# Kernel tuning notes

Measured on AMD Instinct MI355X. Metric: run time of the kernel, lower is better.

The kernel has to match this reference:

```python
import jax, jax.numpy as jnp
import numpy as np

B_SZ, N_NODES, C_IN, C_OUT, M_EDGES, DEG = 32, 4096, 64, 64, 64, 256
E_INC = M_EDGES * DEG  # 16384 incidences
NEG_SLOPE = 0.2
MARGIN = 4.2


def setup_inputs() -> dict:
    key = jax.random.key(0)
    k1, k2, k3, k4 = jax.random.split(key, 4)
    x = jax.random.normal(k1, (B_SZ, N_NODES, C_IN), jnp.float32)
    # glorot-ish params
    weight = jax.random.normal(k2, (C_IN, C_OUT), jnp.float32) * (1.0 / np.sqrt(C_IN))
    att = jax.random.normal(k3, (1, 1, 2 * C_OUT), jnp.float32) * 0.1
    node_ids = jax.random.randint(k4, (E_INC,), 0, N_NODES, dtype=jnp.int32)
    edge_ids = jnp.repeat(jnp.arange(M_EDGES, dtype=jnp.int32), DEG)  # sorted, all edges present
    hyperedge_index = jnp.stack([node_ids, edge_ids], axis=0)
    return {"x": x, "weight": weight, "att": att,
            "hyperedge_index": hyperedge_index,
            "num_edges": M_EDGES, "num_nodes": N_NODES}


def _segment_softmax(scores, seg, num_segments):
    m = jax.ops.segment_max(scores, seg, num_segments=num_segments)
    e = jnp.exp(scores - m[seg])
    s = jax.ops.segment_sum(e, seg, num_segments=num_segments)
    return e / s[seg]


def reference(x, weight, att, hyperedge_index, num_edges, num_nodes):
    node_ids = hyperedge_index[0]
    edge_ids = hyperedge_index[1]
    M = num_edges
    N = num_nodes

    xw = jnp.einsum('bnc,cd->bnd', x, weight)       # [B,N,C]
    x1 = jnp.swapaxes(xw, 0, 1)                     # [N,B,C]

    x_i = x1[node_ids]                              # [E,B,C] gather per incidence
    edge_sums = jax.ops.segment_sum(x_i, edge_ids, num_segments=M,
                                    indices_are_sorted=True)  # [M,B,C]
    x_j = edge_sums[edge_ids]                       # [E,B,C]

    # pairwise hyperedge contrastive loss (vectorized double loop over edges)
    inner = jnp.einsum('kbc,mbc->kmb', edge_sums, edge_sums)          # [M,M,B]
    nrm = jnp.linalg.norm(edge_sums, axis=-1)                         # [M,B]
    cos = inner / (nrm[:, None, :] * nrm[None, :, :])                 # [M,M,B]
    diff = edge_sums[:, None] - edge_sums[None, :]                    # [M,M,B,C]
    dist = jnp.linalg.norm(diff, axis=-1)                             # [M,M,B]
    loss_item = cos * dist + (1.0 - cos) * jnp.clip(MARGIN - dist, 0.0)
    loss_hyper = jnp.sum(jnp.abs(jnp.mean(loss_item, axis=2))) / (M + 1) ** 2

    # GAT-style attention over incidences, softmax grouped by node
    cat = jnp.concatenate([x_i, x_j], axis=-1)                        # [E,B,2C]
    scores = jnp.sum(cat * att[0], axis=-1)                           # [E,B] (heads=1)
    scores = jax.nn.leaky_relu(scores, negative_slope=NEG_SLOPE)
    alpha = _segment_softmax(scores, node_ids, N)                     # [E,B]
    # dropout omitted (eval mode)

    ones = jnp.ones((node_ids.shape[0],), xw.dtype)
    D = jax.ops.segment_sum(ones, node_ids, num_segments=N)           # node degree
    deg_e = jax.ops.segment_sum(ones, edge_ids, num_segments=M, indices_are_sorted=True)
    B_norm = jnp.where(deg_e > 0, 1.0 / deg_e, 0.0)                   # 1/edge degree, inf->0

    # stage 1: nodes -> hyperedges (source_to_target)
    msg1 = B_norm[edge_ids][:, None, None] * (alpha[..., None] * x_i) # [E,B,C]
    out_e = jax.ops.segment_sum(msg1, edge_ids, num_segments=M, indices_are_sorted=True)
    # stage 2: hyperedges -> nodes (target_to_source)
    msg2 = D[node_ids][:, None, None] * (alpha[..., None] * out_e[edge_ids])
    out_n = jax.ops.segment_sum(msg2, node_ids, num_segments=N)       # [N,B,C]

    out = jnp.swapaxes(out_n, 0, 1)                                   # [B,N,C]
    constrain_total = jnp.abs(jnp.mean(x_i - x_j)) + loss_hyper
    return out, constrain_total
```

## Files before the change

### kernel.cpp

```cpp
#include <hip/hip_runtime.h>
#include <math.h>

#define B_SZ 32
#define N_NODES 4096
#define C_DIM 64
#define M_EDGES 64
#define DEG 256
#define E_INC 16384
#define NEG_SLOPE 0.2f
#define MARGIN 4.2f

__device__ __forceinline__ float wsum64(float v) {
#pragma unroll
  for (int off = 32; off > 0; off >>= 1) v += __shfl_xor(v, off, 64);
  return v;
}

__device__ __forceinline__ float4 redq16_32(float4 a) {
#pragma unroll
  for (int off = 16; off < 64; off <<= 1) {
    a.x += __shfl_xor(a.x, off, 64);
    a.y += __shfl_xor(a.y, off, 64);
    a.z += __shfl_xor(a.z, off, 64);
    a.w += __shfl_xor(a.w, off, 64);
  }
  return a;
}

union U16K {
  float wl[4096];
  int cnt[4096];
};

__global__ __launch_bounds__(256) void k_p1(
    const float* __restrict__ x, const float* __restrict__ w,
    const float* __restrict__ att, const int* __restrict__ node_ids,
    float* __restrict__ s1_t, float* __restrict__ es_t,
    float* __restrict__ s2, float* __restrict__ nrm2,
    float* __restrict__ essum, int* __restrict__ cntv) {
  __shared__ U16K u;
  __shared__ float sx[4][64];
  __shared__ float part2[4][64];
  const int bid = blockIdx.x;
  const int t = threadIdx.x;
  if (bid < 2048) {
    const int b = 4 * (bid & 7) + ((bid >> 3) & 3);
    const int m = bid >> 5;
    const int lane = t & 63, wv = t >> 6;
    const int qc = lane & 15, rsub = lane >> 4;
    float4* wl4 = (float4*)u.wl;
    const float4* w4 = (const float4*)w;
#pragma unroll
    for (int i = 0; i < 4; ++i) wl4[t + 256 * i] = w4[t + 256 * i];
    const float4* xb4 = (const float4*)(x + (size_t)b * (N_NODES * C_DIM));
    const int myinc = node_ids[m * DEG + wv * 64 + lane];
    float4 acc = {0.f, 0.f, 0.f, 0.f};
#pragma unroll
    for (int h = 0; h < 2; ++h) {
      int nds[8];
#pragma unroll
      for (int j = 0; j < 8; ++j)
        nds[j] = __shfl(myinc, (h * 8 + j) * 4 + rsub, 64);
      float4 xv[8];
#pragma unroll
      for (int j = 0; j < 8; ++j) xv[j] = xb4[nds[j] * 16 + qc];
#pragma unroll
      for (int j = 0; j < 8; ++j) {
        acc.x += xv[j].x;
        acc.y += xv[j].y;
        acc.z += xv[j].z;
        acc.w += xv[j].w;
      }
    }
    acc = redq16_32(acc);
    if (rsub == 0) ((float4*)sx[wv])[qc] = acc;
    __syncthreads();
    {
      const int c = t & 63;
      float ep = 0.f;
#pragma unroll
      for (int jj = 0; jj < 16; ++jj) {
        const int j = wv * 16 + jj;
        const float sxcj = sx[0][j] + sx[1][j] + sx[2][j] + sx[3][j];
        ep = fmaf(sxcj, u.wl[j * 64 + c], ep);
      }
      part2[wv][c] = ep;
    }
    __syncthreads();
    if (t < 64) {
      const float es = part2[0][t] + part2[1][t] + part2[2][t] + part2[3][t];
      es_t[(m * 64 + t) * 32 + b] = es;
      const float sr = wsum64(es * att[64 + t]);
      const float nr = wsum64(es * es);
      const float er = wsum64(es);
      if (t == 0) {
        s2[m * 32 + b] = sr;
        nrm2[m * 32 + b] = nr;
        essum[m * 32 + b] = er;
      }
    }
  } else if (bid < 2112) {
    const int m = bid - 2048;
#pragma unroll
    for (int i = 0; i < 16; ++i) u.cnt[t + 256 * i] = 0;
    __syncthreads();
    atomicAdd(&u.cnt[node_ids[m * DEG + t]], 1);
    __syncthreads();
#pragma unroll
    for (int i = 0; i < 16; ++i)
      cntv[m * N_NODES + t + 256 * i] = u.cnt[t + 256 * i];
  } else {
    __shared__ float part[4][64];
    __shared__ float wattl[64];
    const int sb = bid - 2112;
    const int kk = t & 63, q = t >> 6;
    float p = 0.f;
#pragma unroll
    for (int c = 0; c < 16; ++c)
      p = fmaf(w[kk * 64 + q * 16 + c], att[q * 16 + c], p);
    part[q][kk] = p;
    __syncthreads();
    if (t < 64)
      wattl[t] = part[0][t] + part[1][t] + part[2][t] + part[3][t];
    __syncthreads();
    const int lane = t & 63, wv = t >> 6;
    const int kq = lane & 15, rsub = lane >> 4;
    const float4 wq = ((const float4*)wattl)[kq];
    const int r0 = sb * 256 + wv * 64;
#pragma unroll 4
    for (int it = 0; it < 16; ++it) {
      const int row = r0 + it * 4 + rsub;
      const float4 xv = ((const float4*)x)[row * 16 + kq];
      float vv = xv.x * wq.x + xv.y * wq.y + xv.z * wq.z + xv.w * wq.w;
      vv += __shfl_xor(vv, 1, 64);
      vv += __shfl_xor(vv, 2, 64);
      vv += __shfl_xor(vv, 4, 64);
      vv += __shfl_xor(vv, 8, 64);
      if (kq == 0) {
        const int n = row & (N_NODES - 1);
        const int b = row >> 12;
        s1_t[n * 32 + b] = vv;
      }
    }
  }
}

__global__ __launch_bounds__(256) void k_p2(
    const float* __restrict__ es_t, const float* __restrict__ nrm2,
    const int* __restrict__ cntv, const float* __restrict__ s1_t,
    const float* __restrict__ s2, float* __restrict__ lossbuf2,
    float2* __restrict__ pnb, int* __restrict__ pdat,
    int* __restrict__ plen) {
  const int bid = blockIdx.x;
  if (bid < 504) {
    const int wv = threadIdx.x >> 6;
    const int p = bid * 4 + wv;
    int k = 0, off = 0;
    while (off + (63 - k) <= p) {
      off += 63 - k;
      ++k;
    }
    const int m = k + 1 + (p - off);
    const int lane = threadIdx.x & 63;
    const int b = lane & 31, ch = lane >> 5;
    float inner = 0.f;
#pragma unroll 8
    for (int cc = 0; cc < 32; ++cc) {
      const int c = cc + 32 * ch;
      inner = fmaf(es_t[(k * 64 + c) * 32 + b], es_t[(m * 64 + c) * 32 + b],
                   inner);
    }
    inner += __shfl_xor(inner, 32, 64);
    const float nk2 = nrm2[k * 32 + b];
    const float nm2 = nrm2[m * 32 + b];
    const float d2 = fmaxf(nk2 + nm2 - 2.f * inner, 0.f);
    const float dist = sqrtf(d2);
    const float cosv = inner / sqrtf(nk2 * nm2);
    float li = cosv * dist + (1.f - cosv) * fmaxf(MARGIN - dist, 0.f);
#pragma unroll
    for (int o = 16; o > 0; o >>= 1) li += __shfl_xor(li, o, 64);
    if (lane == 0) lossbuf2[p] = 2.f * fabsf(li * (1.f / 32.f));
  } else {
    const int idx = (bid - 504) * 256 + threadIdx.x;
    const int n = idx >> 5, b = idx & 31;
    const float s1v = s1_t[n * 32 + b];
    const bool leader = (b == 0);
    float mx = -1e30f, S = 0.f;
    int j = 0, Dsum = 0;
#pragma unroll 4
    for (int m = 0; m < 64; ++m) {
      const int cm = cntv[m * N_NODES + n];
      float sc = s1v + s2[m * 32 + b];
      sc = sc > 0.f ? sc : NEG_SLOPE * sc;
      const float scv = (cm > 0) ? sc : -1e30f;
      const float nm = fmaxf(mx, scv);
      S = S * __expf(mx - nm) + (float)cm * __expf(scv - nm);
      mx = nm;
      if (leader) {
        if (cm > 0) {
          pdat[n * 64 + j] = m | (cm << 8);
          ++j;
        }
        Dsum += cm;
      }
    }
    if (leader) plen[n] = j | (Dsum << 7);
    float2 pv;
    pv.x = mx;
    pv.y = (S > 0.f) ? 1.f / S : 0.f;
    pnb[n * 32 + b] = pv;
  }
}

__global__ __launch_bounds__(256) void k_p3(
    const float* __restrict__ x, const int* __restrict__ node_ids,
    const float* __restrict__ w, const float* __restrict__ s1_t,
    const float* __restrict__ s2, const float2* __restrict__ pnb,
    const float* __restrict__ essum, const float* __restrict__ lossbuf2,
    float* __restrict__ out_e_t, float* __restrict__ outs) {
  __shared__ U16K u;
  __shared__ float sx[4][64];
  __shared__ float part2[4][64];
  const int bid = blockIdx.x;
  const int t = threadIdx.x;
  if (bid < 2048) {
    const int b = 4 * (bid & 7) + ((bid >> 3) & 3);
    const int m = bid >> 5;
    const int lane = t & 63, wv = t >> 6;
    const int qc = lane & 15, rsub = lane >> 4;
    float4* wl4 = (float4*)u.wl;
    const float4* w4 = (const float4*)w;
#pragma unroll
    for (int i = 0; i < 4; ++i) wl4[t + 256 * i] = w4[t + 256 * i];
    const float4* xb4 = (const float4*)(x + (size_t)b * (N_NODES * C_DIM));
    const float s2mb = s2[m * 32 + b];
    const int myinc = node_ids[m * DEG + wv * 64 + lane];
    const float s1v = s1_t[myinc * 32 + b];
    const float2 pv = pnb[myinc * 32 + b];
    float scl = s1v + s2mb;
    scl = scl > 0.f ? scl : NEG_SLOPE * scl;
    const float mya = __expf(scl - pv.x) * pv.y;
    float4 acc = {0.f, 0.f, 0.f, 0.f};
#pragma unroll
    for (int h = 0; h < 2; ++h) {
      int nds[8];
      float av[8];
#pragma unroll
      for (int j = 0; j < 8; ++j) {
        const int idx = (h * 8 + j) * 4 + rsub;
        nds[j] = __shfl(myinc, idx, 64);
        av[j] = __shfl(mya, idx, 64);
      }
      float4 xv[8];
#pragma unroll
      for (int j = 0; j < 8; ++j) xv[j] = xb4[nds[j] * 16 + qc];
#pragma unroll
      for (int j = 0; j < 8; ++j) {
        acc.x = fmaf(av[j], xv[j].x, acc.x);
        acc.y = fmaf(av[j], xv[j].y, acc.y);
        acc.z = fmaf(av[j], xv[j].z, acc.z);
        acc.w = fmaf(av[j], xv[j].w, acc.w);
      }
    }
    acc = redq16_32(acc);
    if (rsub == 0) ((float4*)sx[wv])[qc] = acc;
    __syncthreads();
    {
      const int c = t & 63;
      float ep = 0.f;
#pragma unroll
      for (int jj = 0; jj < 16; ++jj) {
        const int j = wv * 16 + jj;
        const float sxcj = sx[0][j] + sx[1][j] + sx[2][j] + sx[3][j];
        ep = fmaf(sxcj, u.wl[j * 64 + c], ep);
      }
      part2[wv][c] = ep;
    }
    __syncthreads();
    if (t < 64) {
      const float oc =
          part2[0][t] + part2[1][t] + part2[2][t] + part2[3][t];
      out_e_t[(m * 64 + t) * 32 + b] = oc * (1.0f / 256.0f);
    }
  } else {
    __shared__ float smf[256];
    float s = 0.f;
    for (int i = t; i < M_EDGES * B_SZ; i += 256) s += essum[i];
    smf[t] = s;
    __syncthreads();
    for (int o = 128; o > 0; o >>= 1) {
      if (t < o) smf[t] += smf[t + o];
      __syncthreads();
    }
    const float S = smf[0];
    __syncthreads();
    float l = 0.f;
    for (int i = t; i < 2016; i += 256) l += lossbuf2[i];
    smf[t] = l;
    __syncthreads();
    for (int o = 128; o > 0; o >>= 1) {
      if (t < o) smf[t] += smf[t + o];
      __syncthreads();
    }
    if (t == 0) {
      const float mean = S * (-255.0f) / 33554432.0f;
      outs[0] = fabsf(mean) + smf[0] * (1.0f / 4225.0f);
    }
  }
}

__global__ __launch_bounds__(256) void k_p4(
    const int* __restrict__ plen, const int* __restrict__ pdat,
    const float* __restrict__ s1_t, const float* __restrict__ s2,
    const float2* __restrict__ pnb, const float* __restrict__ out_e_t,
    float* __restrict__ out) {
  __shared__ int lme[64];
  __shared__ float lcnt[64];
  __shared__ float al[64][32];
  const int n = blockIdx.x;
  const int t = threadIdx.x;
  const int pl = plen[n];
  const int len = pl & 127;
  const float Dn = (float)(pl >> 7);
  const int c = t & 63, bq = t >> 6;
  const size_t nb = (size_t)n * 64 + c;
  const size_t st = (size_t)N_NODES * 64;
  if (len == 0) {
#pragma unroll
    for (int j = 0; j < 8; ++j) out[(bq * 8 + j) * st + nb] = 0.f;
    return;
  }
  if (t < len) {
    const int pe = pdat[n * 64 + t];
    lme[t] = pe & 63;
    lcnt[t] = (float)(pe >> 8);
  }
  __syncthreads();
  {
    const int b = t & 31, lq = t >> 5;
    const float s1v = s1_t[n * 32 + b];
    const float2 pv = pnb[n * 32 + b];
    for (int base = 0; base < len; base += 8) {
      const int li = base + lq;
      if (li < len) {
        const int m = lme[li];
        float sc = s1v + s2[m * 32 + b];
        sc = sc > 0.f ? sc : NEG_SLOPE * sc;
        al[li][b] = lcnt[li] * __expf(sc - pv.x) * pv.y;
      }
    }
  }
  __syncthreads();
  float4 a0 = {0.f, 0.f, 0.f, 0.f}, a1 = {0.f, 0.f, 0.f, 0.f};
  for (int li = 0; li < len; ++li) {
    const int m = lme[li];
    const float4 v0 = *(const float4*)&out_e_t[(m * 64 + c) * 32 + bq * 8];
    const float4 v1 = *(const float4*)&out_e_t[(m * 64 + c) * 32 + bq * 8 + 4];
    const float* alr = al[li];
    a0.x = fmaf(alr[bq * 8 + 0], v0.x, a0.x);
    a0.y = fmaf(alr[bq * 8 + 1], v0.y, a0.y);
    a0.z = fmaf(alr[bq * 8 + 2], v0.z, a0.z);
    a0.w = fmaf(alr[bq * 8 + 3], v0.w, a0.w);
    a1.x = fmaf(alr[bq * 8 + 4], v1.x, a1.x);
    a1.y = fmaf(alr[bq * 8 + 5], v1.y, a1.y);
    a1.z = fmaf(alr[bq * 8 + 6], v1.z, a1.z);
    a1.w = fmaf(alr[bq * 8 + 7], v1.w, a1.w);
  }
  out[(bq * 8 + 0) * st + nb] = Dn * a0.x;
  out[(bq * 8 + 1) * st + nb] = Dn * a0.y;
  out[(bq * 8 + 2) * st + nb] = Dn * a0.z;
  out[(bq * 8 + 3) * st + nb] = Dn * a0.w;
  out[(bq * 8 + 4) * st + nb] = Dn * a1.x;
  out[(bq * 8 + 5) * st + nb] = Dn * a1.y;
  out[(bq * 8 + 6) * st + nb] = Dn * a1.z;
  out[(bq * 8 + 7) * st + nb] = Dn * a1.w;
}

extern "C" void kernel_launch(void* const* d_in, const int* in_sizes, int n_in,
                              void* d_out, int out_size, void* d_ws,
                              size_t ws_size, hipStream_t stream) {
  (void)in_sizes; (void)n_in; (void)out_size; (void)ws_size;
  const float* x = (const float*)d_in[0];
  const float* weight = (const float*)d_in[1];
  const float* att = (const float*)d_in[2];
  const int* node_ids = (const int*)d_in[3];
  float* out = (float*)d_out;

  char* wsb = (char*)d_ws;
  float* es_t = (float*)(wsb);
  float* out_e_t = (float*)(wsb + (512 << 10));
  float* s1_t = (float*)(wsb + (1024 << 10));
  int* cntv = (int*)(wsb + (1536 << 10));
  float2* pnb = (float2*)(wsb + (2560 << 10));
  int* pdat = (int*)(wsb + (3584 << 10));
  float* s2 = (float*)(wsb + (4608 << 10));
  float* nrm2 = (float*)(wsb + (4616 << 10));
  float* essum = (float*)(wsb + (4624 << 10));
  float* lossbuf2 = (float*)(wsb + (4632 << 10));
  int* plen = (int*)(wsb + (4640 << 10));

  k_p1<<<2624, 256, 0, stream>>>(x, weight, att, node_ids, s1_t, es_t, s2,
                                 nrm2, essum, cntv);
  k_p2<<<1016, 256, 0, stream>>>(es_t, nrm2, cntv, s1_t, s2, lossbuf2, pnb,
                                 pdat, plen);
  k_p3<<<2049, 256, 0, stream>>>(x, node_ids, weight, s1_t, s2, pnb, essum,
                                 lossbuf2, out_e_t,
                                 out + (size_t)B_SZ * N_NODES * C_DIM);
  k_p4<<<4096, 256, 0, stream>>>(plen, pdat, s1_t, s2, pnb, out_e_t, out);
}
```

Baseline: 90.33 us.

## Convert x to fp16 once and gather half-precision rows in edge kernels

Adds a new first kernel that computes the s1 scores, writes an fp16 copy of x into workspace, and builds the per-edge node counts. The two gather kernels (edge sums and attention-weighted edge aggregation) then read 16-byte fp16 chunks of 8 channels instead of fp32 float4s, halving gathered bytes, and use a new lane mapping and shuffle reduction. This costs an extra kernel launch and a full pass writing the fp16 copy, and reduces the precision of gathered inputs, which affects the outputs and the loss accuracy.

```diff
diff --git a/kernel.cpp b/kernel.cpp
--- a/kernel.cpp
+++ b/kernel.cpp
@@ -1,4 +1,5 @@
 #include <hip/hip_runtime.h>
+#include <hip/hip_fp16.h>
 #include <math.h>
 
 #define B_SZ 32
@@ -16,103 +17,16 @@
   return v;
 }
 
-__device__ __forceinline__ float4 redq16_32(float4 a) {
-#pragma unroll
-  for (int off = 16; off < 64; off <<= 1) {
-    a.x += __shfl_xor(a.x, off, 64);
-    a.y += __shfl_xor(a.y, off, 64);
-    a.z += __shfl_xor(a.z, off, 64);
-    a.w += __shfl_xor(a.w, off, 64);
-  }
-  return a;
-}
-
-union U16K {
-  float wl[4096];
-  int cnt[4096];
-};
-
-__global__ __launch_bounds__(256) void k_p1(
+__global__ __launch_bounds__(256) void k_p0(
     const float* __restrict__ x, const float* __restrict__ w,
     const float* __restrict__ att, const int* __restrict__ node_ids,
-    float* __restrict__ s1_t, float* __restrict__ es_t,
-    float* __restrict__ s2, float* __restrict__ nrm2,
-    float* __restrict__ essum, int* __restrict__ cntv) {
-  __shared__ U16K u;
-  __shared__ float sx[4][64];
-  __shared__ float part2[4][64];
+    float* __restrict__ s1_t, __half* __restrict__ xh,
+    int* __restrict__ cntv) {
   const int bid = blockIdx.x;
   const int t = threadIdx.x;
-  if (bid < 2048) {
-    const int b = 4 * (bid & 7) + ((bid >> 3) & 3);
-    const int m = bid >> 5;
-    const int lane = t & 63, wv = t >> 6;
-    const int qc = lane & 15, rsub = lane >> 4;
-    float4* wl4 = (float4*)u.wl;
-    const float4* w4 = (const float4*)w;
-#pragma unroll
-    for (int i = 0; i < 4; ++i) wl4[t + 256 * i] = w4[t + 256 * i];
-    const float4* xb4 = (const float4*)(x + (size_t)b * (N_NODES * C_DIM));
-    const int myinc = node_ids[m * DEG + wv * 64 + lane];
-    float4 acc = {0.f, 0.f, 0.f, 0.f};
-#pragma unroll
-    for (int h = 0; h < 2; ++h) {
-      int nds[8];
-#pragma unroll
-      for (int j = 0; j < 8; ++j)
-        nds[j] = __shfl(myinc, (h * 8 + j) * 4 + rsub, 64);
-      float4 xv[8];
-#pragma unroll
-      for (int j = 0; j < 8; ++j) xv[j] = xb4[nds[j] * 16 + qc];
-#pragma unroll
-      for (int j = 0; j < 8; ++j) {
-        acc.x += xv[j].x;
-        acc.y += xv[j].y;
-        acc.z += xv[j].z;
-        acc.w += xv[j].w;
-      }
-    }
-    acc = redq16_32(acc);
-    if (rsub == 0) ((float4*)sx[wv])[qc] = acc;
-    __syncthreads();
-    {
-      const int c = t & 63;
-      float ep = 0.f;
-#pragma unroll
-      for (int jj = 0; jj < 16; ++jj) {
-        const int j = wv * 16 + jj;
-        const float sxcj = sx[0][j] + sx[1][j] + sx[2][j] + sx[3][j];
-        ep = fmaf(sxcj, u.wl[j * 64 + c], ep);
-      }
-      part2[wv][c] = ep;
-    }
-    __syncthreads();
-    if (t < 64) {
-      const float es = part2[0][t] + part2[1][t] + part2[2][t] + part2[3][t];
-      es_t[(m * 64 + t) * 32 + b] = es;
-      const float sr = wsum64(es * att[64 + t]);
-      const float nr = wsum64(es * es);
-      const float er = wsum64(es);
-      if (t == 0) {
-        s2[m * 32 + b] = sr;
-        nrm2[m * 32 + b] = nr;
-        essum[m * 32 + b] = er;
-      }
-    }
-  } else if (bid < 2112) {
-    const int m = bid - 2048;
-#pragma unroll
-    for (int i = 0; i < 16; ++i) u.cnt[t + 256 * i] = 0;
-    __syncthreads();
-    atomicAdd(&u.cnt[node_ids[m * DEG + t]], 1);
-    __syncthreads();
-#pragma unroll
-    for (int i = 0; i < 16; ++i)
-      cntv[m * N_NODES + t + 256 * i] = u.cnt[t + 256 * i];
-  } else {
+  if (bid < 1024) {
     __shared__ float part[4][64];
     __shared__ float wattl[64];
-    const int sb = bid - 2112;
     const int kk = t & 63, q = t >> 6;
     float p = 0.f;
 #pragma unroll
@@ -126,9 +40,9 @@
     const int lane = t & 63, wv = t >> 6;
     const int kq = lane & 15, rsub = lane >> 4;
     const float4 wq = ((const float4*)wattl)[kq];
-    const int r0 = sb * 256 + wv * 64;
+    const int r0 = bid * 128 + wv * 32;
 #pragma unroll 4
-    for (int it = 0; it < 16; ++it) {
+    for (int it = 0; it < 8; ++it) {
       const int row = r0 + it * 4 + rsub;
       const float4 xv = ((const float4*)x)[row * 16 + kq];
       float vv = xv.x * wq.x + xv.y * wq.y + xv.z * wq.z + xv.w * wq.w;
@@ -141,6 +55,99 @@
         const int b = row >> 12;
         s1_t[n * 32 + b] = vv;
       }
+      union {
+        __half2 h2[2];
+        uint2 u;
+      } pk;
+      pk.h2[0] = __halves2half2(__float2half(xv.x), __float2half(xv.y));
+      pk.h2[1] = __halves2half2(__float2half(xv.z), __float2half(xv.w));
+      ((uint2*)xh)[row * 16 + kq] = pk.u;
+    }
+  } else {
+    __shared__ int cnt[N_NODES];
+    const int m = bid - 1024;
+#pragma unroll
+    for (int i = 0; i < 16; ++i) cnt[t + 256 * i] = 0;
+    __syncthreads();
+    atomicAdd(&cnt[node_ids[m * DEG + t]], 1);
+    __syncthreads();
+#pragma unroll
+    for (int i = 0; i < 16; ++i)
+      cntv[m * N_NODES + t + 256 * i] = cnt[t + 256 * i];
+  }
+}
+
+__global__ __launch_bounds__(256) void k_p1(
+    const __half* __restrict__ xh, const float* __restrict__ w,
+    const float* __restrict__ att, const int* __restrict__ node_ids,
+    float* __restrict__ es_t, float* __restrict__ s2,
+    float* __restrict__ nrm2, float* __restrict__ essum) {
+  __shared__ float wl[4096];
+  __shared__ float sx[4][64];
+  __shared__ float part2[4][64];
+  const int bid = blockIdx.x;
+  const int t = threadIdx.x;
+  const int b = 4 * (bid & 7) + ((bid >> 3) & 3);
+  const int m = bid >> 5;
+  const int lane = t & 63, wv = t >> 6;
+  const int co = lane & 7, rg = lane >> 3;
+  float4* wl4 = (float4*)wl;
+  const float4* w4 = (const float4*)w;
+#pragma unroll
+  for (int i = 0; i < 4; ++i) wl4[t + 256 * i] = w4[t + 256 * i];
+  const uint4* xb = (const uint4*)(xh + (size_t)b * (N_NODES * C_DIM));
+  const int myinc = node_ids[m * DEG + wv * 64 + lane];
+  int nds[8];
+#pragma unroll
+  for (int j = 0; j < 8; ++j) nds[j] = __shfl(myinc, j * 8 + rg, 64);
+  uint4 v[8];
+#pragma unroll
+  for (int j = 0; j < 8; ++j) v[j] = xb[nds[j] * 8 + co];
+  float acc[8] = {0.f, 0.f, 0.f, 0.f, 0.f, 0.f, 0.f, 0.f};
+#pragma unroll
+  for (int j = 0; j < 8; ++j) {
+    const __half2* hp = (const __half2*)&v[j];
+#pragma unroll
+    for (int q = 0; q < 4; ++q) {
+      const float2 f2 = __half22float2(hp[q]);
+      acc[2 * q] += f2.x;
+      acc[2 * q + 1] += f2.y;
+    }
+  }
+#pragma unroll
+  for (int off = 8; off < 64; off <<= 1) {
+#pragma unroll
+    for (int k = 0; k < 8; ++k) acc[k] += __shfl_xor(acc[k], off, 64);
+  }
+  if (rg == 0) {
+    ((float4*)&sx[wv][co * 8])[0] =
+        make_float4(acc[0], acc[1], acc[2], acc[3]);
+    ((float4*)&sx[wv][co * 8])[1] =
+        make_float4(acc[4], acc[5], acc[6], acc[7]);
+  }
+  __syncthreads();
+  {
+    const int c = t & 63;
+    float ep = 0.f;
+#pragma unroll
+    for (int jj = 0; jj < 16; ++jj) {
+      const int j = wv * 16 + jj;
+      const float sxcj = sx[0][j] + sx[1][j] + sx[2][j] + sx[3][j];
+      ep = fmaf(sxcj, wl[j * 64 + c], ep);
+    }
+    part2[wv][c] = ep;
+  }
+  __syncthreads();
+  if (t < 64) {
+    const float es = part2[0][t] + part2[1][t] + part2[2][t] + part2[3][t];
+    es_t[(m * 64 + t) * 32 + b] = es;
+    const float sr = wsum64(es * att[64 + t]);
+    const float nr = wsum64(es * es);
+    const float er = wsum64(es);
+    if (t == 0) {
+      s2[m * 32 + b] = sr;
+      nrm2[m * 32 + b] = nr;
+      essum[m * 32 + b] = er;
     }
   }
 }
@@ -213,12 +220,12 @@
 }
 
 __global__ __launch_bounds__(256) void k_p3(
-    const float* __restrict__ x, const int* __restrict__ node_ids,
+    const __half* __restrict__ xh, const int* __restrict__ node_ids,
     const float* __restrict__ w, const float* __restrict__ s1_t,
     const float* __restrict__ s2, const float2* __restrict__ pnb,
     const float* __restrict__ essum, const float* __restrict__ lossbuf2,
     float* __restrict__ out_e_t, float* __restrict__ outs) {
-  __shared__ U16K u;
+  __shared__ float wl[4096];
   __shared__ float sx[4][64];
   __shared__ float part2[4][64];
   const int bid = blockIdx.x;
@@ -227,12 +234,12 @@
     const int b = 4 * (bid & 7) + ((bid >> 3) & 3);
     const int m = bid >> 5;
     const int lane = t & 63, wv = t >> 6;
-    const int qc = lane & 15, rsub = lane >> 4;
-    float4* wl4 = (float4*)u.wl;
+    const int co = lane & 7, rg = lane >> 3;
+    float4* wl4 = (float4*)wl;
     const float4* w4 = (const float4*)w;
 #pragma unroll
     for (int i = 0; i < 4; ++i) wl4[t + 256 * i] = w4[t + 256 * i];
-    const float4* xb4 = (const float4*)(x + (size_t)b * (N_NODES * C_DIM));
+    const uint4* xb = (const uint4*)(xh + (size_t)b * (N_NODES * C_DIM));
     const float s2mb = s2[m * 32 + b];
     const int myinc = node_ids[m * DEG + wv * 64 + lane];
     const float s1v = s1_t[myinc * 32 + b];
@@ -240,30 +247,38 @@
     float scl = s1v + s2mb;
     scl = scl > 0.f ? scl : NEG_SLOPE * scl;
     const float mya = __expf(scl - pv.x) * pv.y;
-    float4 acc = {0.f, 0.f, 0.f, 0.f};
-#pragma unroll
-    for (int h = 0; h < 2; ++h) {
-      int nds[8];
-      float av[8];
-#pragma unroll
-      for (int j = 0; j < 8; ++j) {
-        const int idx = (h * 8 + j) * 4 + rsub;
-        nds[j] = __shfl(myinc, idx, 64);
-        av[j] = __shfl(mya, idx, 64);
+    int nds[8];
+    float av[8];
+#pragma unroll
+    for (int j = 0; j < 8; ++j) {
+      nds[j] = __shfl(myinc, j * 8 + rg, 64);
+      av[j] = __shfl(mya, j * 8 + rg, 64);
+    }
+    uint4 v[8];
+#pragma unroll
+    for (int j = 0; j < 8; ++j) v[j] = xb[nds[j] * 8 + co];
+    float acc[8] = {0.f, 0.f, 0.f, 0.f, 0.f, 0.f, 0.f, 0.f};
+#pragma unroll
+    for (int j = 0; j < 8; ++j) {
+      const __half2* hp = (const __half2*)&v[j];
+#pragma unroll
+      for (int q = 0; q < 4; ++q) {
+        const float2 f2 = __half22float2(hp[q]);
+        acc[2 * q] = fmaf(av[j], f2.x, acc[2 * q]);
+        acc[2 * q + 1] = fmaf(av[j], f2.y, acc[2 * q + 1]);
       }
-      float4 xv[8];
-#pragma unroll
-      for (int j = 0; j < 8; ++j) xv[j] = xb4[nds[j] * 16 + qc];
-#pragma unroll
-      for (int j = 0; j < 8; ++j) {
-        acc.x = fmaf(av[j], xv[j].x, acc.x);
-        acc.y = fmaf(av[j], xv[j].y, acc.y);
-        acc.z = fmaf(av[j], xv[j].z, acc.z);
-        acc.w = fmaf(av[j], xv[j].w, acc.w);
-      }
-    }
-    acc = redq16_32(acc);
-    if (rsub == 0) ((float4*)sx[wv])[qc] = acc;
+    }
+#pragma unroll
+    for (int off = 8; off < 64; off <<= 1) {
+#pragma unroll
+      for (int k = 0; k < 8; ++k) acc[k] += __shfl_xor(acc[k], off, 64);
+    }
+    if (rg == 0) {
+      ((float4*)&sx[wv][co * 8])[0] =
+          make_float4(acc[0], acc[1], acc[2], acc[3]);
+      ((float4*)&sx[wv][co * 8])[1] =
+          make_float4(acc[4], acc[5], acc[6], acc[7]);
+    }
     __syncthreads();
     {
       const int c = t & 63;
@@ -272,14 +287,13 @@
       for (int jj = 0; jj < 16; ++jj) {
         const int j = wv * 16 + jj;
         const float sxcj = sx[0][j] + sx[1][j] + sx[2][j] + sx[3][j];
-        ep = fmaf(sxcj, u.wl[j * 64 + c], ep);
+        ep = fmaf(sxcj, wl[j * 64 + c], ep);
       }
       part2[wv][c] = ep;
     }
     __syncthreads();
     if (t < 64) {
-      const float oc =
-          part2[0][t] + part2[1][t] + part2[2][t] + part2[3][t];
+      const float oc = part2[0][t] + part2[1][t] + part2[2][t] + part2[3][t];
       out_e_t[(m * 64 + t) * 32 + b] = oc * (1.0f / 256.0f);
     }
   } else {
@@ -398,12 +412,14 @@
   float* essum = (float*)(wsb + (4624 << 10));
   float* lossbuf2 = (float*)(wsb + (4632 << 10));
   int* plen = (int*)(wsb + (4640 << 10));
-
-  k_p1<<<2624, 256, 0, stream>>>(x, weight, att, node_ids, s1_t, es_t, s2,
-                                 nrm2, essum, cntv);
+  __half* xh = (__half*)(wsb + (5120 << 10));
+
+  k_p0<<<1088, 256, 0, stream>>>(x, weight, att, node_ids, s1_t, xh, cntv);
+  k_p1<<<2048, 256, 0, stream>>>(xh, weight, att, node_ids, es_t, s2, nrm2,
+                                 essum);
   k_p2<<<1016, 256, 0, stream>>>(es_t, nrm2, cntv, s1_t, s2, lossbuf2, pnb,
                                  pdat, plen);
-  k_p3<<<2049, 256, 0, stream>>>(x, node_ids, weight, s1_t, s2, pnb, essum,
+  k_p3<<<2049, 256, 0, stream>>>(xh, node_ids, weight, s1_t, s2, pnb, essum,
                                  lossbuf2, out_e_t,
                                  out + (size_t)B_SZ * N_NODES * C_DIM);
   k_p4<<<4096, 256, 0, stream>>>(plen, pdat, s1_t, s2, pnb, out_e_t, out);
```

New measurement: 88.32 us. -2.2%, faster.
